# Optimization experiments

Hardware: AMD Instinct MI355X
Metric: run time of the kernel (lower is better)

Reference implementation:

```python
import jax, jax.numpy as jnp
import numpy as np

B, C, W, H = 4, 512, 64, 64
DQK = 64


def setup_inputs() -> dict:
    key = jax.random.key(0)
    ks = jax.random.split(key, 8)
    s = 1.0 / np.sqrt(C)
    return {
        "x_s": jax.random.normal(ks[0], (B, C, W, H), jnp.float32),
        "x_t": jax.random.normal(ks[1], (B, C, W, H), jnp.float32),
        "Wq": jax.random.normal(ks[2], (DQK, C), jnp.float32) * s,
        "bq": jnp.zeros((DQK,), jnp.float32),
        "Wk": jax.random.normal(ks[3], (DQK, C), jnp.float32) * s,
        "bk": jnp.zeros((DQK,), jnp.float32),
        "Wv": jax.random.normal(ks[4], (C, C), jnp.float32) * s,
        "bv": jnp.zeros((C,), jnp.float32),
        "gamma": jnp.zeros((1,), jnp.float32),
    }


def reference(x_s, x_t, Wq, bq, Wk, bk, Wv, bv, gamma):
    b, c, w, h = x_t.shape
    n = w * h
    xs = x_s.reshape(b, c, n)  # [B,C,N]
    xt = x_t.reshape(b, c, n)
    # 1x1 convs == channel matmuls
    q = jnp.einsum('dc,bcn->bdn', Wq, xt) + bq[None, :, None]  # [B,64,N]
    k = jnp.einsum('dc,bcn->bdn', Wk, xs) + bk[None, :, None]  # [B,64,N]
    v = jnp.einsum('oc,bcn->bon', Wv, xs) + bv[None, :, None]  # [B,C,N]
    # energy[b,i,j] = <q[:,i], k[:,j]>; softmax over j (keys)
    attn = jax.nn.softmax(jnp.einsum('bdi,bdj->bij', q, k), axis=-1)  # [B,N,N]
    # out = V @ attn^T : out[b,c,i] = sum_j v[b,c,j] * attn[b,i,j]
    out = jnp.einsum('bcj,bij->bci', v, attn).reshape(b, c, w, h)
    return gamma * out + x_s
```

## Files before the change

kernel.cpp:

```cpp
#include <hip/hip_runtime.h>

#define B_ 4
#define C_ 512
#define N_ 4096

typedef __attribute__((ext_vector_type(8))) short short8;
typedef __attribute__((ext_vector_type(4))) short short4v;
typedef __attribute__((ext_vector_type(4))) float float4v;

static __device__ __forceinline__ short bfc(float f) {
  unsigned u = __float_as_uint(f);
  u += 0x7FFFu + ((u >> 16) & 1u);
  return (short)(u >> 16);
}

static __device__ __forceinline__ void bar_lgkm() {
  asm volatile("s_waitcnt lgkmcnt(0)" ::: "memory");
  __builtin_amdgcn_s_barrier();
  asm volatile("" ::: "memory");
}

__global__ __launch_bounds__(256) void proj_kernel(
    const float* __restrict__ xs, const float* __restrict__ xt,
    const float* __restrict__ Wq, const float* __restrict__ bq,
    const float* __restrict__ Wk, const float* __restrict__ bk,
    const float* __restrict__ Wv, const float* __restrict__ bv,
    short* __restrict__ Qt, short* __restrict__ Kpk, short* __restrict__ Vpk)
{
  const int bid = blockIdx.x;
  int mode, b, mt, nt;
  const float *W, *bias, *X;
  if (bid < 128)      { mode = 0; b = bid >> 5;        nt = bid & 31;       mt = 0;            W = Wq; bias = bq; X = xt; }
  else if (bid < 256) { mode = 1; int t = bid - 128; b = t >> 5; nt = t & 31; mt = 0;          W = Wk; bias = bk; X = xs; }
  else                { mode = 2; int t = bid - 256; b = t >> 8; mt = (t >> 5) & 7; nt = t & 31; W = Wv; bias = bv; X = xs; }

  __shared__ short xlds[2][128][40];

  const int tid  = threadIdx.x;
  const int wave = tid >> 6;
  const int lane = tid & 63;
  const int l15  = lane & 15;
  const int g    = lane >> 4;
  const int dbase = mt * 64 + wave * 16;
  const int n0 = nt * 128;
  const float* xb = X + (size_t)b * C_ * N_;

  const int nloc = tid & 127;
  const int svw  = ((nloc ^ (nloc >> 3)) & 3) << 1;
  const int cgh  = tid >> 7;

  float v16[16];
  float4v acc[8];
#pragma unroll
  for (int i = 0; i < 8; ++i) acc[i] = (float4v){0.f, 0.f, 0.f, 0.f};

#define XLOAD(CS) { \
    const int c0_ = (CS) * 32; \
    _Pragma("unroll") \
    for (int it_ = 0; it_ < 4; ++it_) { \
      const int cg_ = it_ * 2 + cgh; \
      const float* xp_ = xb + (size_t)(c0_ + cg_ * 4) * N_ + n0 + nloc; \
      _Pragma("unroll") \
      for (int r_ = 0; r_ < 4; ++r_) v16[it_ * 4 + r_] = xp_[(size_t)r_ * N_]; \
    } }

#define XWRITE(BUF) { \
    _Pragma("unroll") \
    for (int it_ = 0; it_ < 4; ++it_) { \
      const int cg_ = it_ * 2 + cgh; \
      short4v pk_; \
      _Pragma("unroll") \
      for (int r_ = 0; r_ < 4; ++r_) pk_[r_] = bfc(v16[it_ * 4 + r_]); \
      *(short4v*)&xlds[BUF][nloc][(cg_ ^ svw) * 4] = pk_; \
    } }

  XLOAD(0);
  XWRITE(0);

  for (int cs = 0; cs < 16; ++cs) {
    __syncthreads();
    if (cs < 15) XLOAD(cs + 1);
    const int pb = cs & 1;
    const float* wp = W + (size_t)(dbase + l15) * C_ + cs * 32 + g * 8;
    float4v wa = *(const float4v*)wp;
    float4v wb2 = *(const float4v*)(wp + 4);
    short8 af;
    af[0]=bfc(wa.x); af[1]=bfc(wa.y); af[2]=bfc(wa.z); af[3]=bfc(wa.w);
    af[4]=bfc(wb2.x); af[5]=bfc(wb2.y); af[6]=bfc(wb2.z); af[7]=bfc(wb2.w);
#pragma unroll
    for (int ct = 0; ct < 8; ++ct) {
      const int nr = ct * 16 + l15;
      const int svr = (nr ^ (nr >> 3)) & 3;
      short8 bf = *(const short8*)&xlds[pb][nr][(g ^ svr) * 8];
      acc[ct] = __builtin_amdgcn_mfma_f32_16x16x32_bf16(af, bf, acc[ct], 0, 0, 0);
    }
    if (cs < 15) XWRITE((cs + 1) & 1);
  }

  float bv4[4];
#pragma unroll
  for (int r = 0; r < 4; ++r) bv4[r] = bias[dbase + g * 4 + r];

  if (mode == 0) {
#pragma unroll
    for (int ct = 0; ct < 8; ++ct) {
      const int n = n0 + ct * 16 + l15;
      short4v pk;
#pragma unroll
      for (int r = 0; r < 4; ++r) pk[r] = bfc(acc[ct][r] + bv4[r]);
      *(short4v*)(Qt + ((size_t)b * N_ + n) * 64 + dbase + g * 4) = pk;
    }
  } else if (mode == 1) {
#pragma unroll
    for (int ct = 0; ct < 8; ++ct) {
      const int n = n0 + ct * 16 + l15;
      short4v pk;
#pragma unroll
      for (int r = 0; r < 4; ++r) pk[r] = bfc(acc[ct][r] + bv4[r]);
      *(short4v*)(Kpk + (((size_t)b * 2 + (dbase >> 5)) * N_ + n) * 32 + (dbase & 31) + g * 4) = pk;
    }
  } else {
#pragma unroll
    for (int ct = 0; ct < 8; ++ct) {
      const int n = n0 + ct * 16 + l15;
      const int jt = n >> 5, jr = n & 31;
      short* vp = Vpk + ((size_t)(b * 128 + jt) * 512) * 32 + jr;
#pragma unroll
      for (int r = 0; r < 4; ++r)
        vp[(size_t)(dbase + g * 4 + r) * 32] = bfc(acc[ct][r] + bv4[r]);
    }
  }
#undef XLOAD
#undef XWRITE
}

__global__ __launch_bounds__(1024) void flash_kernel(
    const short* __restrict__ Qt, const short* __restrict__ Kpk, const short* __restrict__ Vpk,
    const float* __restrict__ xs, const float* __restrict__ gp, float* __restrict__ out)
{
  const int bid = blockIdx.x;
  const int xcd = bid & 7, slot = bid >> 3;
  const int b  = xcd >> 1;
  const int qt = (xcd & 1) * 32 + slot;
  const int q0 = qt * 64;

  __shared__ float S_lds[64][68];
  __shared__ short P_lds[64][72];
  __shared__ float m_sm[64], l_sm[64], corr_sm[64];

  const int tid = threadIdx.x;
  const int wave = tid >> 6, lane = tid & 63;
  const int l15 = lane & 15, g = lane >> 4;

  if (tid < 64) { m_sm[tid] = -1e30f; l_sm[tid] = 0.f; }

  const int s_rt = wave >> 2;
  const int s_ct = wave & 3;
  const int cb   = wave * 32;

  short8 qf0, qf1;
  {
    const short* qp = Qt + ((size_t)b * N_ + q0 + s_rt * 16 + l15) * 64 + g * 8;
    qf0 = *(const short8*)qp;
    qf1 = *(const short8*)(qp + 32);
  }

  float4v acc[4][2];
#pragma unroll
  for (int i = 0; i < 4; ++i)
#pragma unroll
    for (int j = 0; j < 2; ++j) acc[i][j] = (float4v){0.f,0.f,0.f,0.f};

  const int srow = tid >> 4, ssub = tid & 15;

  const short* kbase  = Kpk + ((size_t)b * 2 * N_ + s_ct * 16 + l15) * 32 + g * 8;
  const short* vbaseA = Vpk + ((size_t)(b * 128) * 512 + cb + l15) * 32 + g * 8;
  const short* vbaseB = vbaseA + (size_t)16 * 32;

#define VLOAD(V00, V01, V10, V11, JT0) { \
    const size_t off_ = (size_t)(JT0) * (512 * 32); \
    V00 = *(const short8*)(vbaseA + off_); \
    V01 = *(const short8*)(vbaseB + off_); \
    V10 = *(const short8*)(vbaseA + off_ + 512 * 32); \
    V11 = *(const short8*)(vbaseB + off_ + 512 * 32); \
  }

#define MFMA_BF16 __builtin_amdgcn_mfma_f32_16x16x32_bf16

#define STEP(VC00, VC01, VC10, VC11, VN00, VN01, VN10, VN11, JS) { \
    const int j0_ = (JS) * 64; \
    VLOAD(VN00, VN01, VN10, VN11, (((JS) + 1) & 63) * 2)    \
    { \
      const short* kp_ = kbase + (size_t)j0_ * 32; \
      short8 kf0_ = *(const short8*)kp_; \
      short8 kf1_ = *(const short8*)(kp_ + (size_t)N_ * 32); \
      float4v s_ = (float4v){0.f, 0.f, 0.f, 0.f}; \
      s_ = MFMA_BF16(qf0, kf0_, s_, 0, 0, 0); \
      s_ = MFMA_BF16(qf1, kf1_, s_, 0, 0, 0); \
      _Pragma("unroll") \
      for (int r_ = 0; r_ < 4; ++r_) \
        S_lds[s_rt * 16 + g * 4 + r_][s_ct * 16 + l15] = s_[r_]; \
    } \
    bar_lgkm(); \
    { \
      float4v sv_ = *(const float4v*)&S_lds[srow][ssub * 4]; \
      float mx_ = fmaxf(fmaxf(sv_.x, sv_.y), fmaxf(sv_.z, sv_.w)); \
      mx_ = fmaxf(mx_, __shfl_xor(mx_, 1)); \
      mx_ = fmaxf(mx_, __shfl_xor(mx_, 2)); \
      mx_ = fmaxf(mx_, __shfl_xor(mx_, 4)); \
      mx_ = fmaxf(mx_, __shfl_xor(mx_, 8)); \
      const float mold_ = m_sm[srow]; \
      const float mnew_ = fmaxf(mold_, mx_); \
      const float p0_ = __expf(sv_.x - mnew_), p1_ = __expf(sv_.y - mnew_); \
      const float p2_ = __expf(sv_.z - mnew_), p3_ = __expf(sv_.w - mnew_); \
      short4v pk_; \
      pk_[0] = bfc(p0_); pk_[1] = bfc(p1_); pk_[2] = bfc(p2_); pk_[3] = bfc(p3_); \
      *(short4v*)&P_lds[srow][ssub * 4] = pk_; \
      float ls_ = p0_ + p1_ + p2_ + p3_; \
      ls_ += __shfl_xor(ls_, 1); \
      ls_ += __shfl_xor(ls_, 2); \
      ls_ += __shfl_xor(ls_, 4); \
      ls_ += __shfl_xor(ls_, 8); \
      if (ssub == 0) { \
        const float cr_ = __expf(mold_ - mnew_); \
        l_sm[srow] = l_sm[srow] * cr_ + ls_; \
        m_sm[srow] = mnew_; \
        corr_sm[srow] = cr_; \
      } \
    } \
    bar_lgkm(); \
    { \
      float cr4_[4][4]; \
      int need_ = 0; \
      _Pragma("unroll") \
      for (int rt_ = 0; rt_ < 4; ++rt_) \
        _Pragma("unroll") \
        for (int r_ = 0; r_ < 4; ++r_) { \
          cr4_[rt_][r_] = corr_sm[rt_ * 16 + g * 4 + r_]; \
          need_ |= (cr4_[rt_][r_] != 1.0f); \
        } \
      if (__any(need_)) { \
        _Pragma("unroll") \
        for (int rt_ = 0; rt_ < 4; ++rt_) \
          _Pragma("unroll") \
          for (int ct_ = 0; ct_ < 2; ++ct_) \
            _Pragma("unroll") \
            for (int r_ = 0; r_ < 4; ++r_) acc[rt_][ct_][r_] *= cr4_[rt_][r_]; \
      } \
      __builtin_amdgcn_s_setprio(1); \
      _Pragma("unroll") \
      for (int kt_ = 0; kt_ < 2; ++kt_) { \
        short8 pa_[4]; \
        _Pragma("unroll") \
        for (int rt_ = 0; rt_ < 4; ++rt_) \
          pa_[rt_] = *(const short8*)&P_lds[rt_ * 16 + l15][kt_ * 32 + g * 8]; \
        const short8 vb0_ = kt_ ? VC10 : VC00; \
        const short8 vb1_ = kt_ ? VC11 : VC01; \
        _Pragma("unroll") \
        for (int rt_ = 0; rt_ < 4; ++rt_) { \
          acc[rt_][0] = MFMA_BF16(pa_[rt_], vb0_, acc[rt_][0], 0, 0, 0); \
          acc[rt_][1] = MFMA_BF16(pa_[rt_], vb1_, acc[rt_][1], 0, 0, 0); \
        } \
      } \
      __builtin_amdgcn_s_setprio(0); \
    } \
  }

  short8 a00, a01, a10, a11, b00, b01, b10, b11;
  VLOAD(a00, a01, a10, a11, 0)
  __syncthreads();

  for (int js = 0; js < 64; js += 2) {
    STEP(a00, a01, a10, a11, b00, b01, b10, b11, js)
    STEP(b00, b01, b10, b11, a00, a01, a10, a11, js + 1)
  }
#undef STEP
#undef VLOAD

  const float gm = gp[0];
  float sc[4][4];
#pragma unroll
  for (int rt = 0; rt < 4; ++rt)
#pragma unroll
    for (int r = 0; r < 4; ++r) sc[rt][r] = gm / l_sm[rt * 16 + g * 4 + r];
#pragma unroll
  for (int rt = 0; rt < 4; ++rt)
#pragma unroll
    for (int ct = 0; ct < 2; ++ct) {
      const int c = cb + ct * 16 + l15;
      const size_t base = ((size_t)b * C_ + c) * N_ + q0 + rt * 16 + g * 4;
      float4v xv = *(const float4v*)(xs + base);
      float4v o;
#pragma unroll
      for (int r = 0; r < 4; ++r) o[r] = acc[rt][ct][r] * sc[rt][r] + xv[r];
      *(float4v*)(out + base) = o;
    }
}

extern "C" void kernel_launch(void* const* d_in, const int* in_sizes, int n_in,
                              void* d_out, int out_size, void* d_ws, size_t ws_size,
                              hipStream_t stream) {
  const float* xs = (const float*)d_in[0];
  const float* xt = (const float*)d_in[1];
  const float* Wq = (const float*)d_in[2];
  const float* bq = (const float*)d_in[3];
  const float* Wk = (const float*)d_in[4];
  const float* bk = (const float*)d_in[5];
  const float* Wv = (const float*)d_in[6];
  const float* bv = (const float*)d_in[7];
  const float* gm = (const float*)d_in[8];
  float* out = (float*)d_out;

  char* ws = (char*)d_ws;
  short* Qt  = (short*)(ws);
  short* Kpk = (short*)(ws + (size_t)(2 << 20));
  short* Vpk = (short*)(ws + (size_t)(4 << 20));

  hipLaunchKernelGGL(proj_kernel, dim3(1280), dim3(256), 0, stream,
                     xs, xt, Wq, bq, Wk, bk, Wv, bv, Qt, Kpk, Vpk);
  hipLaunchKernelGGL(flash_kernel, dim3(256), dim3(1024), 0, stream,
                     Qt, Kpk, Vpk, xs, gm, out);
}
```

Before: 300.7 us.

## Split flash attention across channel halves and retile projection for register blocking

The flash kernel now launches 512 blocks of 512 threads. Each block covers one 64-query tile and one half of the 512 value channels, so each wave computes two score tiles and the softmax row reduction uses 8 lanes per row. The projection kernel uses 64-column tiles with 64-channel k-steps, and its V path computes a 64x64 register tile per wave so each loaded X fragment feeds four MFMAs. The aim is more concurrent blocks and better reuse in the projection. The cost is that QK^T and the softmax are recomputed twice per query tile, once for each channel half.

```diff
diff --git a/kernel.cpp b/kernel.cpp
--- a/kernel.cpp
+++ b/kernel.cpp
@@ -20,7 +20,9 @@
   asm volatile("" ::: "memory");
 }
 
-__global__ __launch_bounds__(256) void proj_kernel(
+#define MFMA_BF16 __builtin_amdgcn_mfma_f32_16x16x32_bf16
+
+__global__ __launch_bounds__(256, 4) void proj_kernel(
     const float* __restrict__ xs, const float* __restrict__ xt,
     const float* __restrict__ Wq, const float* __restrict__ bq,
     const float* __restrict__ Wk, const float* __restrict__ bk,
@@ -30,119 +32,146 @@
   const int bid = blockIdx.x;
   int mode, b, mt, nt;
   const float *W, *bias, *X;
-  if (bid < 128)      { mode = 0; b = bid >> 5;        nt = bid & 31;       mt = 0;            W = Wq; bias = bq; X = xt; }
-  else if (bid < 256) { mode = 1; int t = bid - 128; b = t >> 5; nt = t & 31; mt = 0;          W = Wk; bias = bk; X = xs; }
-  else                { mode = 2; int t = bid - 256; b = t >> 8; mt = (t >> 5) & 7; nt = t & 31; W = Wv; bias = bv; X = xs; }
-
-  __shared__ short xlds[2][128][40];
+  if (bid < 256)      { mode = 0; b = bid >> 6;              nt = bid & 63; mt = 0;  W = Wq; bias = bq; X = xt; }
+  else if (bid < 512) { mode = 1; int t = bid - 256; b = t >> 6; nt = t & 63; mt = 0; W = Wk; bias = bk; X = xs; }
+  else                { mode = 2; int t = bid - 512; b = t >> 7; mt = (t >> 6) & 1; nt = t & 63; W = Wv; bias = bv; X = xs; }
+
+  __shared__ short xlds[2][64][72];
 
   const int tid  = threadIdx.x;
   const int wave = tid >> 6;
   const int lane = tid & 63;
   const int l15  = lane & 15;
   const int g    = lane >> 4;
-  const int dbase = mt * 64 + wave * 16;
-  const int n0 = nt * 128;
+  const int n0   = nt * 64;
   const float* xb = X + (size_t)b * C_ * N_;
 
-  const int nloc = tid & 127;
-  const int svw  = ((nloc ^ (nloc >> 3)) & 3) << 1;
-  const int cgh  = tid >> 7;
+  const int nloc = tid & 63;
+  const int cq   = tid >> 6;
 
   float v16[16];
-  float4v acc[8];
-#pragma unroll
-  for (int i = 0; i < 8; ++i) acc[i] = (float4v){0.f, 0.f, 0.f, 0.f};
 
 #define XLOAD(CS) { \
-    const int c0_ = (CS) * 32; \
+    const float* xp_ = xb + (size_t)((CS) * 64 + cq * 16) * N_ + n0 + nloc; \
     _Pragma("unroll") \
-    for (int it_ = 0; it_ < 4; ++it_) { \
-      const int cg_ = it_ * 2 + cgh; \
-      const float* xp_ = xb + (size_t)(c0_ + cg_ * 4) * N_ + n0 + nloc; \
-      _Pragma("unroll") \
-      for (int r_ = 0; r_ < 4; ++r_) v16[it_ * 4 + r_] = xp_[(size_t)r_ * N_]; \
-    } }
+    for (int i_ = 0; i_ < 16; ++i_) v16[i_] = xp_[(size_t)i_ * N_]; \
+  }
 
 #define XWRITE(BUF) { \
     _Pragma("unroll") \
-    for (int it_ = 0; it_ < 4; ++it_) { \
-      const int cg_ = it_ * 2 + cgh; \
-      short4v pk_; \
-      _Pragma("unroll") \
-      for (int r_ = 0; r_ < 4; ++r_) pk_[r_] = bfc(v16[it_ * 4 + r_]); \
-      *(short4v*)&xlds[BUF][nloc][(cg_ ^ svw) * 4] = pk_; \
+    for (int h_ = 0; h_ < 2; ++h_) { \
+      short8 pk_; \
+      _Pragma("unroll") \
+      for (int j_ = 0; j_ < 8; ++j_) pk_[j_] = bfc(v16[h_ * 8 + j_]); \
+      *(short8*)&xlds[BUF][nloc][cq * 16 + h_ * 8] = pk_; \
     } }
 
   XLOAD(0);
   XWRITE(0);
 
-  for (int cs = 0; cs < 16; ++cs) {
-    __syncthreads();
-    if (cs < 15) XLOAD(cs + 1);
-    const int pb = cs & 1;
-    const float* wp = W + (size_t)(dbase + l15) * C_ + cs * 32 + g * 8;
-    float4v wa = *(const float4v*)wp;
-    float4v wb2 = *(const float4v*)(wp + 4);
-    short8 af;
-    af[0]=bfc(wa.x); af[1]=bfc(wa.y); af[2]=bfc(wa.z); af[3]=bfc(wa.w);
-    af[4]=bfc(wb2.x); af[5]=bfc(wb2.y); af[6]=bfc(wb2.z); af[7]=bfc(wb2.w);
-#pragma unroll
-    for (int ct = 0; ct < 8; ++ct) {
-      const int nr = ct * 16 + l15;
-      const int svr = (nr ^ (nr >> 3)) & 3;
-      short8 bf = *(const short8*)&xlds[pb][nr][(g ^ svr) * 8];
-      acc[ct] = __builtin_amdgcn_mfma_f32_16x16x32_bf16(af, bf, acc[ct], 0, 0, 0);
-    }
-    if (cs < 15) XWRITE((cs + 1) & 1);
-  }
-
-  float bv4[4];
-#pragma unroll
-  for (int r = 0; r < 4; ++r) bv4[r] = bias[dbase + g * 4 + r];
-
-  if (mode == 0) {
-#pragma unroll
-    for (int ct = 0; ct < 8; ++ct) {
-      const int n = n0 + ct * 16 + l15;
+  if (mode < 2) {
+    const int dbase = wave * 16;
+    float4v acc[4];
+#pragma unroll
+    for (int i = 0; i < 4; ++i) acc[i] = (float4v){0.f, 0.f, 0.f, 0.f};
+
+    for (int cs = 0; cs < 8; ++cs) {
+      __syncthreads();
+      if (cs < 7) XLOAD(cs + 1);
+      const int pb = cs & 1;
+#pragma unroll
+      for (int kk = 0; kk < 2; ++kk) {
+        const float* wp = W + (size_t)(dbase + l15) * C_ + cs * 64 + kk * 32 + g * 8;
+        float4v wa = *(const float4v*)wp;
+        float4v wb = *(const float4v*)(wp + 4);
+        short8 af;
+        af[0]=bfc(wa.x); af[1]=bfc(wa.y); af[2]=bfc(wa.z); af[3]=bfc(wa.w);
+        af[4]=bfc(wb.x); af[5]=bfc(wb.y); af[6]=bfc(wb.z); af[7]=bfc(wb.w);
+#pragma unroll
+        for (int ns = 0; ns < 4; ++ns) {
+          short8 bf = *(const short8*)&xlds[pb][ns * 16 + l15][kk * 32 + g * 8];
+          acc[ns] = MFMA_BF16(af, bf, acc[ns], 0, 0, 0);
+        }
+      }
+      if (cs < 7) XWRITE((cs + 1) & 1);
+    }
+
+    float bv4[4];
+#pragma unroll
+    for (int r = 0; r < 4; ++r) bv4[r] = bias[dbase + g * 4 + r];
+#pragma unroll
+    for (int ns = 0; ns < 4; ++ns) {
+      const int n = n0 + ns * 16 + l15;
       short4v pk;
 #pragma unroll
-      for (int r = 0; r < 4; ++r) pk[r] = bfc(acc[ct][r] + bv4[r]);
-      *(short4v*)(Qt + ((size_t)b * N_ + n) * 64 + dbase + g * 4) = pk;
-    }
-  } else if (mode == 1) {
-#pragma unroll
-    for (int ct = 0; ct < 8; ++ct) {
-      const int n = n0 + ct * 16 + l15;
-      short4v pk;
-#pragma unroll
-      for (int r = 0; r < 4; ++r) pk[r] = bfc(acc[ct][r] + bv4[r]);
-      *(short4v*)(Kpk + (((size_t)b * 2 + (dbase >> 5)) * N_ + n) * 32 + (dbase & 31) + g * 4) = pk;
+      for (int r = 0; r < 4; ++r) pk[r] = bfc(acc[ns][r] + bv4[r]);
+      if (mode == 0)
+        *(short4v*)(Qt + ((size_t)b * N_ + n) * 64 + dbase + g * 4) = pk;
+      else
+        *(short4v*)(Kpk + (((size_t)b * 2 + (dbase >> 5)) * N_ + n) * 32 + (dbase & 31) + g * 4) = pk;
     }
   } else {
-#pragma unroll
-    for (int ct = 0; ct < 8; ++ct) {
-      const int n = n0 + ct * 16 + l15;
-      const int jt = n >> 5, jr = n & 31;
-      short* vp = Vpk + ((size_t)(b * 128 + jt) * 512) * 32 + jr;
-#pragma unroll
-      for (int r = 0; r < 4; ++r)
-        vp[(size_t)(dbase + g * 4 + r) * 32] = bfc(acc[ct][r] + bv4[r]);
+    const int dbase = mt * 256 + wave * 64;
+    float4v acc[4][4];
+#pragma unroll
+    for (int i = 0; i < 4; ++i)
+#pragma unroll
+      for (int j = 0; j < 4; ++j) acc[i][j] = (float4v){0.f, 0.f, 0.f, 0.f};
+
+    for (int cs = 0; cs < 8; ++cs) {
+      __syncthreads();
+      if (cs < 7) XLOAD(cs + 1);
+      const int pb = cs & 1;
+#pragma unroll
+      for (int kk = 0; kk < 2; ++kk) {
+        short8 af[4];
+#pragma unroll
+        for (int dt = 0; dt < 4; ++dt) {
+          const float* wp = W + (size_t)(dbase + dt * 16 + l15) * C_ + cs * 64 + kk * 32 + g * 8;
+          float4v wa = *(const float4v*)wp;
+          float4v wb = *(const float4v*)(wp + 4);
+          af[dt][0]=bfc(wa.x); af[dt][1]=bfc(wa.y); af[dt][2]=bfc(wa.z); af[dt][3]=bfc(wa.w);
+          af[dt][4]=bfc(wb.x); af[dt][5]=bfc(wb.y); af[dt][6]=bfc(wb.z); af[dt][7]=bfc(wb.w);
+        }
+#pragma unroll
+        for (int ns = 0; ns < 4; ++ns) {
+          short8 bf = *(const short8*)&xlds[pb][ns * 16 + l15][kk * 32 + g * 8];
+#pragma unroll
+          for (int dt = 0; dt < 4; ++dt)
+            acc[dt][ns] = MFMA_BF16(af[dt], bf, acc[dt][ns], 0, 0, 0);
+        }
+      }
+      if (cs < 7) XWRITE((cs + 1) & 1);
+    }
+
+#pragma unroll
+    for (int dt = 0; dt < 4; ++dt) {
+      float bv4[4];
+#pragma unroll
+      for (int r = 0; r < 4; ++r) bv4[r] = bias[dbase + dt * 16 + g * 4 + r];
+#pragma unroll
+      for (int ns = 0; ns < 4; ++ns) {
+        const int n = n0 + ns * 16 + l15;
+        const int jt = n >> 5, jr = n & 31;
+        short* vp = Vpk + (((size_t)b * 128 + jt) * 512 + dbase + dt * 16 + g * 4) * 32 + jr;
+#pragma unroll
+        for (int r = 0; r < 4; ++r) vp[(size_t)r * 32] = bfc(acc[dt][ns][r] + bv4[r]);
+      }
     }
   }
 #undef XLOAD
 #undef XWRITE
 }
 
-__global__ __launch_bounds__(1024) void flash_kernel(
+__global__ __launch_bounds__(512, 4) void flash_kernel(
     const short* __restrict__ Qt, const short* __restrict__ Kpk, const short* __restrict__ Vpk,
     const float* __restrict__ xs, const float* __restrict__ gp, float* __restrict__ out)
 {
   const int bid = blockIdx.x;
   const int xcd = bid & 7, slot = bid >> 3;
-  const int b  = xcd >> 1;
-  const int qt = (xcd & 1) * 32 + slot;
-  const int q0 = qt * 64;
+  const int b     = xcd >> 1;
+  const int chalf = xcd & 1;
+  const int q0    = slot * 64;
 
   __shared__ float S_lds[64][68];
   __shared__ short P_lds[64][72];
@@ -154,9 +183,9 @@
 
   if (tid < 64) { m_sm[tid] = -1e30f; l_sm[tid] = 0.f; }
 
-  const int s_rt = wave >> 2;
-  const int s_ct = wave & 3;
-  const int cb   = wave * 32;
+  const int s_rt  = wave >> 1;
+  const int s_ct0 = (wave & 1) * 2;
+  const int cb    = chalf * 256 + wave * 32;
 
   short8 qf0, qf1;
   {
@@ -171,9 +200,9 @@
 #pragma unroll
     for (int j = 0; j < 2; ++j) acc[i][j] = (float4v){0.f,0.f,0.f,0.f};
 
-  const int srow = tid >> 4, ssub = tid & 15;
-
-  const short* kbase  = Kpk + ((size_t)b * 2 * N_ + s_ct * 16 + l15) * 32 + g * 8;
+  const int srow = tid >> 3, ssub = tid & 7;
+
+  const short* kbase  = Kpk + ((size_t)b * 2 * N_ + s_ct0 * 16 + l15) * 32 + g * 8;
   const short* vbaseA = Vpk + ((size_t)(b * 128) * 512 + cb + l15) * 32 + g * 8;
   const short* vbaseB = vbaseA + (size_t)16 * 32;
 
@@ -185,13 +214,12 @@
     V11 = *(const short8*)(vbaseB + off_ + 512 * 32); \
   }
 
-#define MFMA_BF16 __builtin_amdgcn_mfma_f32_16x16x32_bf16
-
 #define STEP(VC00, VC01, VC10, VC11, VN00, VN01, VN10, VN11, JS) { \
     const int j0_ = (JS) * 64; \
     VLOAD(VN00, VN01, VN10, VN11, (((JS) + 1) & 63) * 2)    \
-    { \
-      const short* kp_ = kbase + (size_t)j0_ * 32; \
+    _Pragma("unroll") \
+    for (int t_ = 0; t_ < 2; ++t_) { \
+      const short* kp_ = kbase + ((size_t)j0_ + t_ * 16) * 32; \
       short8 kf0_ = *(const short8*)kp_; \
       short8 kf1_ = *(const short8*)(kp_ + (size_t)N_ * 32); \
       float4v s_ = (float4v){0.f, 0.f, 0.f, 0.f}; \
@@ -199,28 +227,30 @@
       s_ = MFMA_BF16(qf1, kf1_, s_, 0, 0, 0); \
       _Pragma("unroll") \
       for (int r_ = 0; r_ < 4; ++r_) \
-        S_lds[s_rt * 16 + g * 4 + r_][s_ct * 16 + l15] = s_[r_]; \
+        S_lds[s_rt * 16 + g * 4 + r_][(s_ct0 + t_) * 16 + l15] = s_[r_]; \
     } \
     bar_lgkm(); \
     { \
-      float4v sv_ = *(const float4v*)&S_lds[srow][ssub * 4]; \
-      float mx_ = fmaxf(fmaxf(sv_.x, sv_.y), fmaxf(sv_.z, sv_.w)); \
+      float4v s0_ = *(const float4v*)&S_lds[srow][ssub * 8]; \
+      float4v s1_ = *(const float4v*)&S_lds[srow][ssub * 8 + 4]; \
+      float mx_ = fmaxf(fmaxf(fmaxf(s0_.x, s0_.y), fmaxf(s0_.z, s0_.w)), \
+                        fmaxf(fmaxf(s1_.x, s1_.y), fmaxf(s1_.z, s1_.w))); \
       mx_ = fmaxf(mx_, __shfl_xor(mx_, 1)); \
       mx_ = fmaxf(mx_, __shfl_xor(mx_, 2)); \
       mx_ = fmaxf(mx_, __shfl_xor(mx_, 4)); \
-      mx_ = fmaxf(mx_, __shfl_xor(mx_, 8)); \
       const float mold_ = m_sm[srow]; \
       const float mnew_ = fmaxf(mold_, mx_); \
-      const float p0_ = __expf(sv_.x - mnew_), p1_ = __expf(sv_.y - mnew_); \
-      const float p2_ = __expf(sv_.z - mnew_), p3_ = __expf(sv_.w - mnew_); \
-      short4v pk_; \
-      pk_[0] = bfc(p0_); pk_[1] = bfc(p1_); pk_[2] = bfc(p2_); pk_[3] = bfc(p3_); \
-      *(short4v*)&P_lds[srow][ssub * 4] = pk_; \
-      float ls_ = p0_ + p1_ + p2_ + p3_; \
+      float p_[8]; \
+      p_[0]=__expf(s0_.x-mnew_); p_[1]=__expf(s0_.y-mnew_); p_[2]=__expf(s0_.z-mnew_); p_[3]=__expf(s0_.w-mnew_); \
+      p_[4]=__expf(s1_.x-mnew_); p_[5]=__expf(s1_.y-mnew_); p_[6]=__expf(s1_.z-mnew_); p_[7]=__expf(s1_.w-mnew_); \
+      short8 pk_; \
+      _Pragma("unroll") \
+      for (int r_ = 0; r_ < 8; ++r_) pk_[r_] = bfc(p_[r_]); \
+      *(short8*)&P_lds[srow][ssub * 8] = pk_; \
+      float ls_ = p_[0]+p_[1]+p_[2]+p_[3]+p_[4]+p_[5]+p_[6]+p_[7]; \
       ls_ += __shfl_xor(ls_, 1); \
       ls_ += __shfl_xor(ls_, 2); \
       ls_ += __shfl_xor(ls_, 4); \
-      ls_ += __shfl_xor(ls_, 8); \
       if (ssub == 0) { \
         const float cr_ = __expf(mold_ - mnew_); \
         l_sm[srow] = l_sm[srow] * cr_ + ls_; \
@@ -230,15 +260,14 @@
     } \
     bar_lgkm(); \
     { \
-      float cr4_[4][4]; \
+      float4v cr4_[4]; \
       int need_ = 0; \
       _Pragma("unroll") \
-      for (int rt_ = 0; rt_ < 4; ++rt_) \
-        _Pragma("unroll") \
-        for (int r_ = 0; r_ < 4; ++r_) { \
-          cr4_[rt_][r_] = corr_sm[rt_ * 16 + g * 4 + r_]; \
-          need_ |= (cr4_[rt_][r_] != 1.0f); \
-        } \
+      for (int rt_ = 0; rt_ < 4; ++rt_) { \
+        cr4_[rt_] = *(const float4v*)&corr_sm[rt_ * 16 + g * 4]; \
+        need_ |= (cr4_[rt_][0] != 1.0f) | (cr4_[rt_][1] != 1.0f) | \
+                 (cr4_[rt_][2] != 1.0f) | (cr4_[rt_][3] != 1.0f); \
+      } \
       if (__any(need_)) { \
         _Pragma("unroll") \
         for (int rt_ = 0; rt_ < 4; ++rt_) \
@@ -280,9 +309,11 @@
   const float gm = gp[0];
   float sc[4][4];
 #pragma unroll
-  for (int rt = 0; rt < 4; ++rt)
-#pragma unroll
-    for (int r = 0; r < 4; ++r) sc[rt][r] = gm / l_sm[rt * 16 + g * 4 + r];
+  for (int rt = 0; rt < 4; ++rt) {
+    float4v lv = *(const float4v*)&l_sm[rt * 16 + g * 4];
+#pragma unroll
+    for (int r = 0; r < 4; ++r) sc[rt][r] = gm / lv[r];
+  }
 #pragma unroll
   for (int rt = 0; rt < 4; ++rt)
 #pragma unroll
@@ -316,8 +347,8 @@
   short* Kpk = (short*)(ws + (size_t)(2 << 20));
   short* Vpk = (short*)(ws + (size_t)(4 << 20));
 
-  hipLaunchKernelGGL(proj_kernel, dim3(1280), dim3(256), 0, stream,
+  hipLaunchKernelGGL(proj_kernel, dim3(1024), dim3(256), 0, stream,
                      xs, xt, Wq, bq, Wk, bk, Wv, bv, Qt, Kpk, Vpk);
-  hipLaunchKernelGGL(flash_kernel, dim3(256), dim3(1024), 0, stream,
+  hipLaunchKernelGGL(flash_kernel, dim3(512), dim3(512), 0, stream,
                      Qt, Kpk, Vpk, xs, gm, out);
 }
```

After: 303.6 us. No clear change (+1.0%).
